# Kernel optimization log

Measured on AMD Instinct MI355X. Metric: run time of the kernel, lower is better.

## Reference

```python
import jax, jax.numpy as jnp
import numpy as np

I, H = 512, 1024

def setup_inputs() -> dict:
    key = jax.random.key(0)
    ks = jax.random.split(key, 5)
    s_ih = 1.0 / np.sqrt(I)
    s_hh = 1.0 / np.sqrt(H)
    return {
        "x": jax.random.normal(ks[0], (512, 64, I), dtype=jnp.float32),
        "W_ih": jax.random.uniform(ks[1], (4 * H, I), minval=-s_ih, maxval=s_ih, dtype=jnp.float32),
        "b_ih": jax.random.uniform(ks[2], (4 * H,), minval=-s_ih, maxval=s_ih, dtype=jnp.float32),
        "W_hh": jax.random.uniform(ks[3], (4 * H, H), minval=-s_hh, maxval=s_hh, dtype=jnp.float32),
        "b_hh": jax.random.uniform(ks[4], (4 * H,), minval=-s_hh, maxval=s_hh, dtype=jnp.float32),
    }

def _lstm(x, W_ih, b_ih, W_hh, b_hh):
    T, B, _ = x.shape
    Hh = W_hh.shape[1]
    # Precompute input projection for all timesteps: [T, B, 4H]
    x_proj = jnp.einsum("tbi,gi->tbg", x, W_ih) + b_ih + b_hh

    def step(carry, xp):
        h, c = carry
        gates = xp + h @ W_hh.T  # [B, 4H]
        i_g, f_g, g_g, o_g = jnp.split(gates, 4, axis=1)
        i_g = jax.nn.sigmoid(i_g)
        f_g = jax.nn.sigmoid(f_g)
        g_g = jnp.tanh(g_g)
        o_g = jax.nn.sigmoid(o_g)
        c = f_g * c + i_g * g_g
        h = o_g * jnp.tanh(c)
        return (h, c), h

    h0 = jnp.zeros((B, Hh), dtype=x.dtype)
    c0 = jnp.zeros((B, Hh), dtype=x.dtype)
    (hT, cT), out = jax.lax.scan(step, (h0, c0), x_proj)
    return out, (hT, cT)

def reference(x, W_ih, b_ih, W_hh, b_hh):
    out, (hT, cT) = _lstm(x, W_ih, b_ih, W_hh, b_hh)
    return out, hT, cT
```

## Files before the change

### kernel.cpp

```cpp
#include <hip/hip_runtime.h>

#define T_STEPS 512
#define BATCH   64
#define IN      512
#define HID     1024
#define GDIM    4096
#define MROWS   (T_STEPS * BATCH)
#define RING    64
#define SENTW   0x7F7F7F7Fu

typedef __attribute__((ext_vector_type(8))) short bf16x8_t;
typedef __attribute__((ext_vector_type(4))) float f32x4_t;

__device__ __forceinline__ unsigned short f2bf(float f) {
  union { float f; unsigned int u; } v; v.f = f;
  unsigned int r = v.u + 0x7FFFu + ((v.u >> 16) & 1u);
  return (unsigned short)(r >> 16);
}
__device__ __forceinline__ float bf2f(unsigned short u) {
  union { unsigned int u; float f; } v; v.u = ((unsigned int)u) << 16;
  return v.f;
}
__device__ __forceinline__ float sigmoidf_(float x) {
  return 1.0f / (1.0f + __expf(-x));
}
__device__ __forceinline__ float tanhf_(float x) {
  return 1.0f - 2.0f / (__expf(2.0f * x) + 1.0f);
}
__device__ __forceinline__ f32x4_t MFMA_(bf16x8_t a, bf16x8_t b, f32x4_t c) {
  return __builtin_amdgcn_mfma_f32_16x16x32_bf16(a, b, c, 0, 0, 0);
}

__global__ void k_cvt(const float* __restrict__ src, unsigned short* __restrict__ dst, int n) {
  int i = (blockIdx.x * blockDim.x + threadIdx.x) * 4;
  if (i + 3 < n) {
    float4 f = *(const float4*)(src + i);
    ushort4 o;
    o.x = f2bf(f.x); o.y = f2bf(f.y); o.z = f2bf(f.z); o.w = f2bf(f.w);
    *(ushort4*)(dst + i) = o;
  }
}

__global__ void k_bias(const float* __restrict__ a, const float* __restrict__ b,
                       float* __restrict__ o) {
  int i = blockIdx.x * blockDim.x + threadIdx.x;
  if (i < GDIM) o[i] = a[i] + b[i];
}

__global__ __launch_bounds__(256) void k_xproj(
    const float* __restrict__ x,
    const unsigned short* __restrict__ Wih,
    const float* __restrict__ bias,
    unsigned short* __restrict__ xproj)
{
  const int AP = 40;
  __shared__ unsigned short Alds[128 * AP];
  __shared__ unsigned short Blds[128 * AP];
  const int tid = threadIdx.x;
  const int w = tid >> 6, l = tid & 63;
  const int m0 = blockIdx.y * 128, n0 = blockIdx.x * 128;
  const int wm = (w >> 1) * 64, wn = (w & 1) * 64;
  f32x4_t acc[4][4] = {};

  for (int k0 = 0; k0 < IN; k0 += 32) {
    #pragma unroll
    for (int it = 0; it < 2; ++it) {
      int chunk = tid + it * 256;
      int row = chunk >> 2;
      int kc  = (chunk & 3) * 8;
      const float* src = x + (size_t)(m0 + row) * IN + k0 + kc;
      float4 f0 = *(const float4*)(src);
      float4 f1 = *(const float4*)(src + 4);
      union { bf16x8_t v; unsigned short s[8]; } u;
      u.s[0]=f2bf(f0.x); u.s[1]=f2bf(f0.y); u.s[2]=f2bf(f0.z); u.s[3]=f2bf(f0.w);
      u.s[4]=f2bf(f1.x); u.s[5]=f2bf(f1.y); u.s[6]=f2bf(f1.z); u.s[7]=f2bf(f1.w);
      *(bf16x8_t*)&Alds[row * AP + kc] = u.v;
    }
    #pragma unroll
    for (int it = 0; it < 2; ++it) {
      int chunk = tid + it * 256;
      int row = chunk >> 2;
      int kc  = (chunk & 3) * 8;
      *(bf16x8_t*)&Blds[row * AP + kc] =
          *(const bf16x8_t*)(Wih + (size_t)(n0 + row) * IN + k0 + kc);
    }
    __syncthreads();
    bf16x8_t a[4], b[4];
    #pragma unroll
    for (int i = 0; i < 4; ++i)
      a[i] = *(const bf16x8_t*)&Alds[(wm + i * 16 + (l & 15)) * AP + ((l >> 4) * 8)];
    #pragma unroll
    for (int i = 0; i < 4; ++i)
      b[i] = *(const bf16x8_t*)&Blds[(wn + i * 16 + (l & 15)) * AP + ((l >> 4) * 8)];
    #pragma unroll
    for (int mi = 0; mi < 4; ++mi) {
      #pragma unroll
      for (int ni = 0; ni < 4; ++ni)
        acc[mi][ni] = __builtin_amdgcn_mfma_f32_16x16x32_bf16(a[mi], b[ni], acc[mi][ni], 0, 0, 0);
    }
    __syncthreads();
  }
  #pragma unroll
  for (int ni = 0; ni < 4; ++ni) {
    int col = n0 + wn + ni * 16 + (l & 15);
    float bv = bias[col];
    #pragma unroll
    for (int mi = 0; mi < 4; ++mi) {
      int rbase = m0 + wm + mi * 16 + (l >> 4) * 4;
      #pragma unroll
      for (int r = 0; r < 4; ++r)
        xproj[(size_t)(rbase + r) * GDIM + col] = f2bf(acc[mi][ni][r] + bv);
    }
  }
}

__global__ __launch_bounds__(256, 1) void k_lstm_persist(
    const unsigned short* __restrict__ xproj,
    const unsigned short* __restrict__ Whh,
    unsigned short* __restrict__ ring,
    float* __restrict__ out,
    float* __restrict__ hT,
    float* __restrict__ cT)
{
  __shared__ __align__(16) unsigned short Hlds[16384];
  __shared__ float Glds[4][8][33];

  const int tid = threadIdx.x;
  const int w = tid >> 6, l = tid & 63;
  const int grp  = blockIdx.x >> 5;
  const int slot = blockIdx.x & 31;
  const int b0 = grp * 8, n0 = slot * 32;

  {
    bf16x8_t zv = {0, 0, 0, 0, 0, 0, 0, 0};
    #pragma unroll
    for (int i = 0; i < 8; ++i)
      *(bf16x8_t*)((char*)Hlds + (size_t)(i * 256 + tid) * 16) = zv;
  }
  __syncthreads();

  bf16x8_t wf[64];
  {
    const unsigned short* wp0 =
        Whh + (size_t)((w << 10) + n0 + (l & 15)) * HID + ((l >> 4) * 8);
    const unsigned short* wp1 = wp0 + (size_t)16 * HID;
    #pragma unroll
    for (int ks = 0; ks < 32; ++ks) {
      wf[ks]      = *(const bf16x8_t*)(wp0 + ks * 32);
      wf[32 + ks] = *(const bf16x8_t*)(wp1 + ks * 32);
    }
  }

  const int eb = tid >> 5, en = tid & 31;
  const size_t ci = (size_t)(b0 + eb) * HID + n0 + en;
  float creg = 0.0f;

  const int abase = (l & 15) * 2048 + ((l >> 4) * 16);
  const int amask = (l & 7) << 4;

  #pragma unroll 1
  for (int t = 0; t < T_STEPS; ++t) {
    const unsigned short* xpp = xproj + ((size_t)t * BATCH + b0 + eb) * GDIM + n0 + en;
    unsigned short x0 = xpp[0], x1 = xpp[1024], x2 = xpp[2048], x3 = xpp[3072];
    asm volatile("" ::: "memory");

    if (t > 0) {
      const char* rsrc = (const char*)(ring +
          ((size_t)((t - 1) & (RING - 1)) * BATCH + b0) * HID);
      union { bf16x8_t v; unsigned int u[4]; } hv[4];
      unsigned int need = 1u;
      do {
        #pragma unroll
        for (int i = 0; i < 4; ++i) {
          unsigned long long ap = (unsigned long long)(rsrc + (size_t)(i * 256 + tid) * 16);
          asm volatile("global_load_dwordx4 %0, %1, off sc0 sc1"
                       : "=v"(hv[i].v) : "v"(ap) : "memory");
        }
        asm volatile("s_waitcnt vmcnt(0)" ::: "memory");
        unsigned int bad = 0;
        #pragma unroll
        for (int i = 0; i < 4; ++i) {
          bad |= (hv[i].u[0] == SENTW) | (hv[i].u[1] == SENTW);
          bad |= (hv[i].u[2] == SENTW) | (hv[i].u[3] == SENTW);
        }
        need = bad;
        if (need) __builtin_amdgcn_s_sleep(1);
      } while (need);
      __builtin_amdgcn_sched_barrier(0);
      #pragma unroll
      for (int i = 0; i < 4; ++i) {
        int d = (i * 256 + tid) * 16;
        int sd = d ^ (((d >> 11) & 7) << 4);
        *(bf16x8_t*)((char*)Hlds + sd) = hv[i].v;
      }
    }
    __syncthreads();

    f32x4_t ac0 = {0,0,0,0}, ac1 = {0,0,0,0}, ac2 = {0,0,0,0}, ac3 = {0,0,0,0};
    #pragma unroll
    for (int ks = 0; ks < 32; ks += 2) {
      bf16x8_t a0 = *(const bf16x8_t*)((const char*)Hlds + ((abase + (ks+0)*64) ^ amask));
      bf16x8_t a1 = *(const bf16x8_t*)((const char*)Hlds + ((abase + (ks+1)*64) ^ amask));
      ac0 = MFMA_(a0, wf[ks],          ac0);
      ac1 = MFMA_(a0, wf[32 + ks],     ac1);
      ac2 = MFMA_(a1, wf[ks + 1],      ac2);
      ac3 = MFMA_(a1, wf[32 + ks + 1], ac3);
    }
    f32x4_t s0 = ac0 + ac2;
    f32x4_t s1 = ac1 + ac3;

    if ((l >> 4) < 2) {
      int r0 = (l >> 4) * 4, cc = l & 15;
      #pragma unroll
      for (int j = 0; j < 4; ++j) {
        Glds[w][r0 + j][cc]      = s0[j];
        Glds[w][r0 + j][16 + cc] = s1[j];
      }
    }
    __syncthreads();

    float pre0 = Glds[0][eb][en] + bf2f(x0);
    float pre1 = Glds[1][eb][en] + bf2f(x1);
    float pre2 = Glds[2][eb][en] + bf2f(x2);
    float pre3 = Glds[3][eb][en] + bf2f(x3);
    float ig = sigmoidf_(pre0);
    float fg = sigmoidf_(pre1);
    float gg = tanhf_(pre2);
    float og = sigmoidf_(pre3);
    creg = fg * creg + ig * gg;
    float hv = og * tanhf_(creg);

    if (t == T_STEPS - 1) {
      out[((size_t)t * BATCH + b0 + eb) * HID + n0 + en] = hv;
      hT[ci] = hv;
      cT[ci] = creg;
    } else {
      unsigned short mybf = f2bf(hv);
      unsigned short pbf = (unsigned short)(unsigned int)
          __shfl_xor((int)(unsigned int)mybf, 1, 64);
      if ((l & 1) == 0) {
        unsigned int pk = ((unsigned int)mybf) | (((unsigned int)pbf) << 16);
        unsigned short* rdst = ring + (size_t)(t & (RING - 1)) * BATCH * HID;
        __hip_atomic_store((unsigned int*)(rdst + ci), pk,
                           __ATOMIC_RELAXED, __HIP_MEMORY_SCOPE_AGENT);
        unsigned short* rrst = ring + (size_t)((t + 32) & (RING - 1)) * BATCH * HID;
        __hip_atomic_store((unsigned int*)(rrst + ci), SENTW,
                           __ATOMIC_RELAXED, __HIP_MEMORY_SCOPE_AGENT);
      }
      out[((size_t)t * BATCH + b0 + eb) * HID + n0 + en] = hv;
    }
  }
}

__global__ __launch_bounds__(256) void k_step_fused(
    const unsigned short* __restrict__ hprev,
    unsigned short* __restrict__ hnext,
    float* __restrict__ cstate,
    const unsigned short* __restrict__ Whh,
    const unsigned short* __restrict__ Wih,
    const float* __restrict__ x,
    const float* __restrict__ bias,
    float* __restrict__ out,
    float* __restrict__ hT, float* __restrict__ cT,
    int t, int is_last)
{
  const int RS = 1560;
  const int XB = 1032;
  __shared__ unsigned short Hlds[16 * RS];
  __shared__ float Glds[4][16][17];
  const int tid = threadIdx.x;
  const int w = tid >> 6, l = tid & 63;
  const int bg = blockIdx.x >> 6, hs = blockIdx.x & 63;
  const int b0 = bg * 16, n0 = hs * 16;

  #pragma unroll
  for (int it = 0; it < 8; ++it) {
    int chunk = tid + it * 256;
    int row = chunk >> 7;
    int cc  = (chunk & 127) * 8;
    *(bf16x8_t*)&Hlds[row * RS + cc] =
        *(const bf16x8_t*)(hprev + (size_t)(b0 + row) * HID + cc);
  }
  #pragma unroll
  for (int it = 0; it < 4; ++it) {
    int chunk = tid + it * 256;
    int row = chunk >> 6;
    int cc  = (chunk & 63) * 8;
    const float* src = x + ((size_t)t * BATCH + b0 + row) * IN + cc;
    float4 f0 = *(const float4*)(src);
    float4 f1 = *(const float4*)(src + 4);
    union { bf16x8_t v; unsigned short s[8]; } u;
    u.s[0]=f2bf(f0.x); u.s[1]=f2bf(f0.y); u.s[2]=f2bf(f0.z); u.s[3]=f2bf(f0.w);
    u.s[4]=f2bf(f1.x); u.s[5]=f2bf(f1.y); u.s[6]=f2bf(f1.z); u.s[7]=f2bf(f1.w);
    *(bf16x8_t*)&Hlds[row * RS + XB + cc] = u.v;
  }
  __syncthreads();

  f32x4_t acc = {0.f, 0.f, 0.f, 0.f};
  const int gcol = (w << 10) + n0 + (l & 15);
  const unsigned short* wp = Whh + (size_t)gcol * HID + ((l >> 4) * 8);
  const unsigned short* ap = &Hlds[(l & 15) * RS + ((l >> 4) * 8)];
  #pragma unroll 4
  for (int ks = 0; ks < 32; ++ks) {
    bf16x8_t a = *(const bf16x8_t*)(ap);
    bf16x8_t b = *(const bf16x8_t*)(wp);
    acc = __builtin_amdgcn_mfma_f32_16x16x32_bf16(a, b, acc, 0, 0, 0);
    ap += 32; wp += 32;
  }
  const unsigned short* wpx = Wih + (size_t)gcol * IN + ((l >> 4) * 8);
  const unsigned short* apx = &Hlds[(l & 15) * RS + XB + ((l >> 4) * 8)];
  #pragma unroll 4
  for (int ks = 0; ks < 16; ++ks) {
    bf16x8_t a = *(const bf16x8_t*)(apx);
    bf16x8_t b = *(const bf16x8_t*)(wpx);
    acc = __builtin_amdgcn_mfma_f32_16x16x32_bf16(a, b, acc, 0, 0, 0);
    apx += 32; wpx += 32;
  }

  {
    int r0 = (l >> 4) * 4, cc = l & 15;
    Glds[w][r0 + 0][cc] = acc[0];
    Glds[w][r0 + 1][cc] = acc[1];
    Glds[w][r0 + 2][cc] = acc[2];
    Glds[w][r0 + 3][cc] = acc[3];
  }
  __syncthreads();

  int b = tid >> 4, n = tid & 15;
  float pre[4];
  #pragma unroll
  for (int g = 0; g < 4; ++g)
    pre[g] = Glds[g][b][n] + bias[(g << 10) + n0 + n];
  float ig = sigmoidf_(pre[0]);
  float fg = sigmoidf_(pre[1]);
  float gg = tanhf_(pre[2]);
  float og = sigmoidf_(pre[3]);
  size_t ci = (size_t)(b0 + b) * HID + n0 + n;
  float cn = fg * cstate[ci] + ig * gg;
  float hv = og * tanhf_(cn);
  cstate[ci] = cn;
  out[((size_t)t * BATCH + b0 + b) * HID + n0 + n] = hv;
  hnext[ci] = f2bf(hv);
  if (is_last) { hT[ci] = hv; cT[ci] = cn; }
}

extern "C" void kernel_launch(void* const* d_in, const int* in_sizes, int n_in,
                              void* d_out, int out_size, void* d_ws, size_t ws_size,
                              hipStream_t stream) {
  const float* x    = (const float*)d_in[0];
  const float* Wihf = (const float*)d_in[1];
  const float* bih  = (const float*)d_in[2];
  const float* Whhf = (const float*)d_in[3];
  const float* bhh  = (const float*)d_in[4];
  float* out = (float*)d_out;

  char* ws = (char*)d_ws;
  size_t off = 0;
  auto take = [&](size_t bytes) {
    char* p = ws + off;
    off = (off + bytes + 255) & ~(size_t)255;
    return p;
  };
  unsigned short* wih_b = (unsigned short*)take((size_t)GDIM * IN * 2);
  unsigned short* whh_b = (unsigned short*)take((size_t)GDIM * HID * 2);
  float*          bias  = (float*)take((size_t)GDIM * 4);
  unsigned short* h0    = (unsigned short*)take((size_t)BATCH * HID * 2);
  unsigned short* h1    = (unsigned short*)take((size_t)BATCH * HID * 2);
  float*          cbuf  = (float*)take((size_t)BATCH * HID * 4);
  unsigned short* ring  = (unsigned short*)take((size_t)RING * BATCH * HID * 2);
  unsigned short* xproj = (unsigned short*)take((size_t)MROWS * GDIM * 2);
  size_t full_need = off;
  const int primary = (ws_size >= full_need) ? 1 : 0;
  (void)in_sizes; (void)n_in; (void)out_size;

  k_cvt<<<(GDIM * IN / 4 + 255) / 256, 256, 0, stream>>>(Wihf, wih_b, GDIM * IN);
  k_cvt<<<(GDIM * HID / 4 + 255) / 256, 256, 0, stream>>>(Whhf, whh_b, GDIM * HID);
  k_bias<<<(GDIM + 255) / 256, 256, 0, stream>>>(bih, bhh, bias);
  (void)hipMemsetAsync(h0, 0, (size_t)BATCH * HID * 2, stream);

  float* hT = out + (size_t)T_STEPS * BATCH * HID;
  float* cT = hT + (size_t)BATCH * HID;

  if (primary) {
    (void)hipMemsetAsync(ring, 0x7F, (size_t)RING * BATCH * HID * 2, stream);
    k_xproj<<<dim3(GDIM / 128, MROWS / 128), 256, 0, stream>>>(x, wih_b, bias, xproj);
    void* p_xproj = (void*)xproj; void* p_whh = (void*)whh_b;
    void* p_ring = (void*)ring;   void* p_out = (void*)out;
    void* p_hT = (void*)hT;       void* p_cT = (void*)cT;
    void* args[6] = {&p_xproj, &p_whh, &p_ring, &p_out, &p_hT, &p_cT};
    hipError_t err = hipLaunchCooperativeKernel((const void*)k_lstm_persist,
                                                dim3(256), dim3(256), args, 0, stream);
    if (err == hipSuccess) return;
  }

  (void)hipMemsetAsync(cbuf, 0, (size_t)BATCH * HID * 4, stream);
  unsigned short* hp = h0;
  unsigned short* hn = h1;
  for (int t = 0; t < T_STEPS; ++t) {
    int last = (t == T_STEPS - 1) ? 1 : 0;
    k_step_fused<<<256, 256, 0, stream>>>(hp, hn, cbuf, whh_b, wih_b, x, bias,
                                          out, hT, cT, t, last);
    unsigned short* tmp = hp; hp = hn; hn = tmp;
  }
}
```

Measured before the change: 2.042 ms.

## Process two batch groups per persistent block to overlap ring polling with compute

The persistent LSTM kernel now runs 128 blocks instead of 256, and each block handles two 8-row batch groups (A and B) that share the register-resident W_hh slice. After waiting for group A's previous hidden state, the block issues group B's ring loads and computes A's GEMM and gates while those loads are in flight, then validates B and computes it. The aim is to hide cross-block sync latency and halve the number of blocks that poll the ring. The cost is that per-step serial work per block doubles on half as many CUs.

```diff
diff --git a/kernel.cpp b/kernel.cpp
--- a/kernel.cpp
+++ b/kernel.cpp
@@ -96,7 +96,7 @@
     for (int mi = 0; mi < 4; ++mi) {
       #pragma unroll
       for (int ni = 0; ni < 4; ++ni)
-        acc[mi][ni] = __builtin_amdgcn_mfma_f32_16x16x32_bf16(a[mi], b[ni], acc[mi][ni], 0, 0, 0);
+        acc[mi][ni] = MFMA_(a[mi], b[ni], acc[mi][ni]);
     }
     __syncthreads();
   }
@@ -127,9 +127,11 @@
 
   const int tid = threadIdx.x;
   const int w = tid >> 6, l = tid & 63;
-  const int grp  = blockIdx.x >> 5;
+  const int pair = blockIdx.x >> 5;
   const int slot = blockIdx.x & 31;
-  const int b0 = grp * 8, n0 = slot * 32;
+  const int n0  = slot * 32;
+  const int b0A = pair * 16;
+  const int b0B = pair * 16 + 8;
 
   {
     bf16x8_t zv = {0, 0, 0, 0, 0, 0, 0, 0};
@@ -152,46 +154,67 @@
   }
 
   const int eb = tid >> 5, en = tid & 31;
-  const size_t ci = (size_t)(b0 + eb) * HID + n0 + en;
-  float creg = 0.0f;
+  const size_t ciA = (size_t)(b0A + eb) * HID + n0 + en;
+  const size_t ciB = (size_t)(b0B + eb) * HID + n0 + en;
+  float cregA = 0.0f, cregB = 0.0f;
 
   const int abase = (l & 15) * 2048 + ((l >> 4) * 16);
   const int amask = (l & 7) << 4;
 
   #pragma unroll 1
   for (int t = 0; t < T_STEPS; ++t) {
-    const unsigned short* xpp = xproj + ((size_t)t * BATCH + b0 + eb) * GDIM + n0 + en;
-    unsigned short x0 = xpp[0], x1 = xpp[1024], x2 = xpp[2048], x3 = xpp[3072];
+    const unsigned short* xpA = xproj + ((size_t)t * BATCH + b0A + eb) * GDIM + n0 + en;
+    const unsigned short* xpB = xproj + ((size_t)t * BATCH + b0B + eb) * GDIM + n0 + en;
+    unsigned short xA0 = xpA[0], xA1 = xpA[1024], xA2 = xpA[2048], xA3 = xpA[3072];
+    unsigned short xB0 = xpB[0], xB1 = xpB[1024], xB2 = xpB[2048], xB3 = xpB[3072];
     asm volatile("" ::: "memory");
 
+    union HV { bf16x8_t v; unsigned int u[4]; };
+    HV hvB0, hvB1, hvB2, hvB3;
+    const char* rsrcB = (const char*)(ring +
+        ((size_t)((t - 1) & (RING - 1)) * BATCH + b0B) * HID);
+
     if (t > 0) {
-      const char* rsrc = (const char*)(ring +
-          ((size_t)((t - 1) & (RING - 1)) * BATCH + b0) * HID);
-      union { bf16x8_t v; unsigned int u[4]; } hv[4];
+      const char* rsrcA = (const char*)(ring +
+          ((size_t)((t - 1) & (RING - 1)) * BATCH + b0A) * HID);
+      HV hvA0, hvA1, hvA2, hvA3;
       unsigned int need = 1u;
       do {
-        #pragma unroll
-        for (int i = 0; i < 4; ++i) {
-          unsigned long long ap = (unsigned long long)(rsrc + (size_t)(i * 256 + tid) * 16);
-          asm volatile("global_load_dwordx4 %0, %1, off sc0 sc1"
-                       : "=v"(hv[i].v) : "v"(ap) : "memory");
-        }
+        asm volatile("global_load_dwordx4 %0, %1, off sc0 sc1" : "=v"(hvA0.v)
+                     : "v"((unsigned long long)(rsrcA + (size_t)(0 * 256 + tid) * 16)) : "memory");
+        asm volatile("global_load_dwordx4 %0, %1, off sc0 sc1" : "=v"(hvA1.v)
+                     : "v"((unsigned long long)(rsrcA + (size_t)(1 * 256 + tid) * 16)) : "memory");
+        asm volatile("global_load_dwordx4 %0, %1, off sc0 sc1" : "=v"(hvA2.v)
+                     : "v"((unsigned long long)(rsrcA + (size_t)(2 * 256 + tid) * 16)) : "memory");
+        asm volatile("global_load_dwordx4 %0, %1, off sc0 sc1" : "=v"(hvA3.v)
+                     : "v"((unsigned long long)(rsrcA + (size_t)(3 * 256 + tid) * 16)) : "memory");
         asm volatile("s_waitcnt vmcnt(0)" ::: "memory");
         unsigned int bad = 0;
-        #pragma unroll
-        for (int i = 0; i < 4; ++i) {
-          bad |= (hv[i].u[0] == SENTW) | (hv[i].u[1] == SENTW);
-          bad |= (hv[i].u[2] == SENTW) | (hv[i].u[3] == SENTW);
-        }
+        bad |= (hvA0.u[0]==SENTW)|(hvA0.u[1]==SENTW)|(hvA0.u[2]==SENTW)|(hvA0.u[3]==SENTW);
+        bad |= (hvA1.u[0]==SENTW)|(hvA1.u[1]==SENTW)|(hvA1.u[2]==SENTW)|(hvA1.u[3]==SENTW);
+        bad |= (hvA2.u[0]==SENTW)|(hvA2.u[1]==SENTW)|(hvA2.u[2]==SENTW)|(hvA2.u[3]==SENTW);
+        bad |= (hvA3.u[0]==SENTW)|(hvA3.u[1]==SENTW)|(hvA3.u[2]==SENTW)|(hvA3.u[3]==SENTW);
         need = bad;
         if (need) __builtin_amdgcn_s_sleep(1);
       } while (need);
+
+      asm volatile("global_load_dwordx4 %0, %1, off sc0 sc1" : "=v"(hvB0.v)
+                   : "v"((unsigned long long)(rsrcB + (size_t)(0 * 256 + tid) * 16)) : "memory");
+      asm volatile("global_load_dwordx4 %0, %1, off sc0 sc1" : "=v"(hvB1.v)
+                   : "v"((unsigned long long)(rsrcB + (size_t)(1 * 256 + tid) * 16)) : "memory");
+      asm volatile("global_load_dwordx4 %0, %1, off sc0 sc1" : "=v"(hvB2.v)
+                   : "v"((unsigned long long)(rsrcB + (size_t)(2 * 256 + tid) * 16)) : "memory");
+      asm volatile("global_load_dwordx4 %0, %1, off sc0 sc1" : "=v"(hvB3.v)
+                   : "v"((unsigned long long)(rsrcB + (size_t)(3 * 256 + tid) * 16)) : "memory");
+
       __builtin_amdgcn_sched_barrier(0);
-      #pragma unroll
-      for (int i = 0; i < 4; ++i) {
-        int d = (i * 256 + tid) * 16;
-        int sd = d ^ (((d >> 11) & 7) << 4);
-        *(bf16x8_t*)((char*)Hlds + sd) = hv[i].v;
+      {
+        int d0 = (0 * 256 + tid) * 16, d1 = (1 * 256 + tid) * 16;
+        int d2 = (2 * 256 + tid) * 16, d3 = (3 * 256 + tid) * 16;
+        *(bf16x8_t*)((char*)Hlds + (d0 ^ (((d0 >> 11) & 7) << 4))) = hvA0.v;
+        *(bf16x8_t*)((char*)Hlds + (d1 ^ (((d1 >> 11) & 7) << 4))) = hvA1.v;
+        *(bf16x8_t*)((char*)Hlds + (d2 ^ (((d2 >> 11) & 7) << 4))) = hvA2.v;
+        *(bf16x8_t*)((char*)Hlds + (d3 ^ (((d3 >> 11) & 7) << 4))) = hvA3.v;
       }
     }
     __syncthreads();
@@ -206,48 +229,140 @@
       ac2 = MFMA_(a1, wf[ks + 1],      ac2);
       ac3 = MFMA_(a1, wf[32 + ks + 1], ac3);
     }
-    f32x4_t s0 = ac0 + ac2;
-    f32x4_t s1 = ac1 + ac3;
-
-    if ((l >> 4) < 2) {
-      int r0 = (l >> 4) * 4, cc = l & 15;
-      #pragma unroll
-      for (int j = 0; j < 4; ++j) {
-        Glds[w][r0 + j][cc]      = s0[j];
-        Glds[w][r0 + j][16 + cc] = s1[j];
+    {
+      f32x4_t s0 = ac0 + ac2, s1 = ac1 + ac3;
+      if ((l >> 4) < 2) {
+        int r0 = (l >> 4) * 4, cc = l & 15;
+        #pragma unroll
+        for (int j = 0; j < 4; ++j) {
+          Glds[w][r0 + j][cc]      = s0[j];
+          Glds[w][r0 + j][16 + cc] = s1[j];
+        }
       }
     }
     __syncthreads();
 
-    float pre0 = Glds[0][eb][en] + bf2f(x0);
-    float pre1 = Glds[1][eb][en] + bf2f(x1);
-    float pre2 = Glds[2][eb][en] + bf2f(x2);
-    float pre3 = Glds[3][eb][en] + bf2f(x3);
-    float ig = sigmoidf_(pre0);
-    float fg = sigmoidf_(pre1);
-    float gg = tanhf_(pre2);
-    float og = sigmoidf_(pre3);
-    creg = fg * creg + ig * gg;
-    float hv = og * tanhf_(creg);
-
-    if (t == T_STEPS - 1) {
-      out[((size_t)t * BATCH + b0 + eb) * HID + n0 + en] = hv;
-      hT[ci] = hv;
-      cT[ci] = creg;
-    } else {
-      unsigned short mybf = f2bf(hv);
-      unsigned short pbf = (unsigned short)(unsigned int)
-          __shfl_xor((int)(unsigned int)mybf, 1, 64);
-      if ((l & 1) == 0) {
-        unsigned int pk = ((unsigned int)mybf) | (((unsigned int)pbf) << 16);
-        unsigned short* rdst = ring + (size_t)(t & (RING - 1)) * BATCH * HID;
-        __hip_atomic_store((unsigned int*)(rdst + ci), pk,
-                           __ATOMIC_RELAXED, __HIP_MEMORY_SCOPE_AGENT);
-        unsigned short* rrst = ring + (size_t)((t + 32) & (RING - 1)) * BATCH * HID;
-        __hip_atomic_store((unsigned int*)(rrst + ci), SENTW,
-                           __ATOMIC_RELAXED, __HIP_MEMORY_SCOPE_AGENT);
-      }
-      out[((size_t)t * BATCH + b0 + eb) * HID + n0 + en] = hv;
+    if (t > 0) {
+      asm volatile("s_waitcnt vmcnt(0)" ::: "memory");
+      unsigned int bad = 0;
+      bad |= (hvB0.u[0]==SENTW)|(hvB0.u[1]==SENTW)|(hvB0.u[2]==SENTW)|(hvB0.u[3]==SENTW);
+      bad |= (hvB1.u[0]==SENTW)|(hvB1.u[1]==SENTW)|(hvB1.u[2]==SENTW)|(hvB1.u[3]==SENTW);
+      bad |= (hvB2.u[0]==SENTW)|(hvB2.u[1]==SENTW)|(hvB2.u[2]==SENTW)|(hvB2.u[3]==SENTW);
+      bad |= (hvB3.u[0]==SENTW)|(hvB3.u[1]==SENTW)|(hvB3.u[2]==SENTW)|(hvB3.u[3]==SENTW);
+      while (bad) {
+        __builtin_amdgcn_s_sleep(1);
+        asm volatile("global_load_dwordx4 %0, %1, off sc0 sc1" : "=v"(hvB0.v)
+                     : "v"((unsigned long long)(rsrcB + (size_t)(0 * 256 + tid) * 16)) : "memory");
+        asm volatile("global_load_dwordx4 %0, %1, off sc0 sc1" : "=v"(hvB1.v)
+                     : "v"((unsigned long long)(rsrcB + (size_t)(1 * 256 + tid) * 16)) : "memory");
+        asm volatile("global_load_dwordx4 %0, %1, off sc0 sc1" : "=v"(hvB2.v)
+                     : "v"((unsigned long long)(rsrcB + (size_t)(2 * 256 + tid) * 16)) : "memory");
+        asm volatile("global_load_dwordx4 %0, %1, off sc0 sc1" : "=v"(hvB3.v)
+                     : "v"((unsigned long long)(rsrcB + (size_t)(3 * 256 + tid) * 16)) : "memory");
+        asm volatile("s_waitcnt vmcnt(0)" ::: "memory");
+        bad = 0;
+        bad |= (hvB0.u[0]==SENTW)|(hvB0.u[1]==SENTW)|(hvB0.u[2]==SENTW)|(hvB0.u[3]==SENTW);
+        bad |= (hvB1.u[0]==SENTW)|(hvB1.u[1]==SENTW)|(hvB1.u[2]==SENTW)|(hvB1.u[3]==SENTW);
+        bad |= (hvB2.u[0]==SENTW)|(hvB2.u[1]==SENTW)|(hvB2.u[2]==SENTW)|(hvB2.u[3]==SENTW);
+        bad |= (hvB3.u[0]==SENTW)|(hvB3.u[1]==SENTW)|(hvB3.u[2]==SENTW)|(hvB3.u[3]==SENTW);
+      }
+      __builtin_amdgcn_sched_barrier(0);
+      {
+        int d0 = (0 * 256 + tid) * 16, d1 = (1 * 256 + tid) * 16;
+        int d2 = (2 * 256 + tid) * 16, d3 = (3 * 256 + tid) * 16;
+        *(bf16x8_t*)((char*)Hlds + (d0 ^ (((d0 >> 11) & 7) << 4))) = hvB0.v;
+        *(bf16x8_t*)((char*)Hlds + (d1 ^ (((d1 >> 11) & 7) << 4))) = hvB1.v;
+        *(bf16x8_t*)((char*)Hlds + (d2 ^ (((d2 >> 11) & 7) << 4))) = hvB2.v;
+        *(bf16x8_t*)((char*)Hlds + (d3 ^ (((d3 >> 11) & 7) << 4))) = hvB3.v;
+      }
+    }
+
+    {
+      float pre0 = Glds[0][eb][en] + bf2f(xA0);
+      float pre1 = Glds[1][eb][en] + bf2f(xA1);
+      float pre2 = Glds[2][eb][en] + bf2f(xA2);
+      float pre3 = Glds[3][eb][en] + bf2f(xA3);
+      float ig = sigmoidf_(pre0);
+      float fg = sigmoidf_(pre1);
+      float gg = tanhf_(pre2);
+      float og = sigmoidf_(pre3);
+      cregA = fg * cregA + ig * gg;
+      float hv = og * tanhf_(cregA);
+      if (t == T_STEPS - 1) {
+        out[((size_t)t * BATCH + b0A + eb) * HID + n0 + en] = hv;
+        hT[ciA] = hv;
+        cT[ciA] = cregA;
+      } else {
+        unsigned short mybf = f2bf(hv);
+        unsigned short pbf = (unsigned short)(unsigned int)
+            __shfl_xor((int)(unsigned int)mybf, 1, 64);
+        if ((l & 1) == 0) {
+          unsigned int pk = ((unsigned int)mybf) | (((unsigned int)pbf) << 16);
+          unsigned short* rdst = ring + (size_t)(t & (RING - 1)) * BATCH * HID;
+          __hip_atomic_store((unsigned int*)(rdst + ciA), pk,
+                             __ATOMIC_RELAXED, __HIP_MEMORY_SCOPE_AGENT);
+          unsigned short* rrst = ring + (size_t)((t + 32) & (RING - 1)) * BATCH * HID;
+          __hip_atomic_store((unsigned int*)(rrst + ciA), SENTW,
+                             __ATOMIC_RELAXED, __HIP_MEMORY_SCOPE_AGENT);
+        }
+        out[((size_t)t * BATCH + b0A + eb) * HID + n0 + en] = hv;
+      }
+    }
+    __syncthreads();
+
+    f32x4_t bc0 = {0,0,0,0}, bc1 = {0,0,0,0}, bc2 = {0,0,0,0}, bc3 = {0,0,0,0};
+    #pragma unroll
+    for (int ks = 0; ks < 32; ks += 2) {
+      bf16x8_t a0 = *(const bf16x8_t*)((const char*)Hlds + ((abase + (ks+0)*64) ^ amask));
+      bf16x8_t a1 = *(const bf16x8_t*)((const char*)Hlds + ((abase + (ks+1)*64) ^ amask));
+      bc0 = MFMA_(a0, wf[ks],          bc0);
+      bc1 = MFMA_(a0, wf[32 + ks],     bc1);
+      bc2 = MFMA_(a1, wf[ks + 1],      bc2);
+      bc3 = MFMA_(a1, wf[32 + ks + 1], bc3);
+    }
+    {
+      f32x4_t s0 = bc0 + bc2, s1 = bc1 + bc3;
+      if ((l >> 4) < 2) {
+        int r0 = (l >> 4) * 4, cc = l & 15;
+        #pragma unroll
+        for (int j = 0; j < 4; ++j) {
+          Glds[w][r0 + j][cc]      = s0[j];
+          Glds[w][r0 + j][16 + cc] = s1[j];
+        }
+      }
+    }
+    __syncthreads();
+
+    {
+      float pre0 = Glds[0][eb][en] + bf2f(xB0);
+      float pre1 = Glds[1][eb][en] + bf2f(xB1);
+      float pre2 = Glds[2][eb][en] + bf2f(xB2);
+      float pre3 = Glds[3][eb][en] + bf2f(xB3);
+      float ig = sigmoidf_(pre0);
+      float fg = sigmoidf_(pre1);
+      float gg = tanhf_(pre2);
+      float og = sigmoidf_(pre3);
+      cregB = fg * cregB + ig * gg;
+      float hv = og * tanhf_(cregB);
+      if (t == T_STEPS - 1) {
+        out[((size_t)t * BATCH + b0B + eb) * HID + n0 + en] = hv;
+        hT[ciB] = hv;
+        cT[ciB] = cregB;
+      } else {
+        unsigned short mybf = f2bf(hv);
+        unsigned short pbf = (unsigned short)(unsigned int)
+            __shfl_xor((int)(unsigned int)mybf, 1, 64);
+        if ((l & 1) == 0) {
+          unsigned int pk = ((unsigned int)mybf) | (((unsigned int)pbf) << 16);
+          unsigned short* rdst = ring + (size_t)(t & (RING - 1)) * BATCH * HID;
+          __hip_atomic_store((unsigned int*)(rdst + ciB), pk,
+                             __ATOMIC_RELAXED, __HIP_MEMORY_SCOPE_AGENT);
+          unsigned short* rrst = ring + (size_t)((t + 32) & (RING - 1)) * BATCH * HID;
+          __hip_atomic_store((unsigned int*)(rrst + ciB), SENTW,
+                             __ATOMIC_RELAXED, __HIP_MEMORY_SCOPE_AGENT);
+        }
+        out[((size_t)t * BATCH + b0B + eb) * HID + n0 + en] = hv;
+      }
     }
   }
 }
@@ -389,7 +504,7 @@
     void* p_hT = (void*)hT;       void* p_cT = (void*)cT;
     void* args[6] = {&p_xproj, &p_whh, &p_ring, &p_out, &p_hT, &p_cT};
     hipError_t err = hipLaunchCooperativeKernel((const void*)k_lstm_persist,
-                                                dim3(256), dim3(256), args, 0, stream);
+                                                dim3(128), dim3(256), args, 0, stream);
     if (err == hipSuccess) return;
   }
 
```

After: 2.697 ms. 32.1% more time.
